# Kernel tuning notes

Hardware: AMD Instinct MI355X
Metric: run time of the kernel (lower is better)

## Reference

```python
import jax, jax.numpy as jnp
import numpy as np

B, D, N_CLASSES = 8192, 256, 64
MARGIN = 0.5


def setup_inputs() -> dict:
    key = jax.random.key(0)
    k1, k2 = jax.random.split(key)
    emb = jax.random.normal(k1, (B, D), dtype=jnp.float32)
    emb = emb / jnp.linalg.norm(emb, axis=1, keepdims=True)  # module expects L2-normalised
    labels = jax.random.randint(k2, (B,), 0, N_CLASSES)
    return {"embeddings": emb, "labels": labels}


def _pairwise_dist(x):
    # torch.cdist(x, x, p=2): sqrt of clamped squared distances, safe at 0 for grads
    sq = jnp.sum(x * x, axis=1)
    d2 = jnp.maximum(sq[:, None] + sq[None, :] - 2.0 * (x @ x.T), 0.0)
    safe = jnp.where(d2 > 0.0, d2, 1.0)
    return jnp.where(d2 > 0.0, jnp.sqrt(safe), 0.0)


def reference(embeddings, labels):
    # Vectorized semi-hard mining: for each anchor,
    #   d_ap = max positive distance; the mined negative is the MIN negative
    #   distance (argmin over the semi-hard subset == global neg argmin when
    #   that min is < d_ap + margin; otherwise the subset is empty -> skip).
    dist = _pairwise_dist(embeddings)            # [B, B]
    n = labels.shape[0]
    same = labels[:, None] == labels[None, :]
    eye = jnp.eye(n, dtype=bool)
    pos_mask = same & ~eye
    neg_mask = ~same

    NEG = jnp.float32(-1e30)
    POS = jnp.float32(1e30)
    d_ap = jnp.max(jnp.where(pos_mask, dist, NEG), axis=1)   # hardest positive
    d_an = jnp.min(jnp.where(neg_mask, dist, POS), axis=1)   # closest negative

    has_pos = jnp.any(pos_mask, axis=1)
    has_neg = jnp.any(neg_mask, axis=1)
    valid = has_pos & has_neg & (d_an < d_ap + MARGIN)       # semi-hard exists

    losses = jax.nn.relu(d_ap - d_an + MARGIN)
    count = jnp.sum(valid)
    total = jnp.sum(jnp.where(valid, losses, 0.0))
    zero = jnp.sum(embeddings) * 0.0
    return jnp.where(count > 0, total / jnp.maximum(count, 1).astype(losses.dtype), zero)
```

## Files before the change

### kernel.cpp

```cpp
#include <hip/hip_runtime.h>
#include <hip/hip_bf16.h>

#define Bn 8192
#define Dn 256
#define MARGIN_F 0.5f

typedef short short8 __attribute__((ext_vector_type(8)));
typedef float floatx4 __attribute__((ext_vector_type(4)));

__device__ inline unsigned short f2bf(float f) {
    unsigned int u = __float_as_uint(f);
    unsigned int r = (u + 0x7fffu + ((u >> 16) & 1u)) >> 16;
    return (unsigned short)r;
}

#define OFF_SQ   ((size_t)Bn * Dn * 2)
#define OFF_POS  (OFF_SQ + Bn * 4)
#define OFF_NEG  (OFF_POS + Bn * 4)
#define OFF_ACC  (OFF_NEG + Bn * 4)

__global__ __launch_bounds__(256) void prep_kernel(
        const float* __restrict__ emb, unsigned short* __restrict__ embT,
        float* __restrict__ sq, unsigned int* __restrict__ posb,
        unsigned int* __restrict__ negb, unsigned int* __restrict__ accs) {
    const int w = threadIdx.x >> 6;
    const int lane = threadIdx.x & 63;
    const int row = blockIdx.x * 4 + w;

    const float4 v = *(const float4*)(emb + (size_t)row * Dn + lane * 4);
    float ss = v.x * v.x + v.y * v.y + v.z * v.z + v.w * v.w;
    #pragma unroll
    for (int m = 32; m >= 1; m >>= 1) ss += __shfl_xor(ss, m);

    uint2 o;
    o.x = (unsigned int)f2bf(v.x) | ((unsigned int)f2bf(v.y) << 16);
    o.y = (unsigned int)f2bf(v.z) | ((unsigned int)f2bf(v.w) << 16);
    const int kg = lane >> 1;
    *(uint2*)(embT + ((size_t)kg * Bn + row) * 8 + (lane & 1) * 4) = o;

    if (lane == 0) {
        sq[row] = ss;
        posb[row] = 0u;
        negb[row] = 0xFFFFFFFFu;
    }
    if (blockIdx.x == 0 && threadIdx.x == 0) {
        accs[0] = 0u; accs[1] = 0u; accs[2] = 0u;
    }
}

__global__ __launch_bounds__(256, 3) void mine_kernel(
        const unsigned short* __restrict__ embT, const float* __restrict__ sq,
        const int* __restrict__ labels, unsigned int* __restrict__ posb,
        unsigned int* __restrict__ negb) {
    const int tid  = threadIdx.x;
    const int w    = tid >> 6;
    const int lane = tid & 63;
    const int quad = lane >> 4;
    const int c    = lane & 15;

    const int iBase = blockIdx.x * 128 + w * 32;
    const int jBase = blockIdx.y * 512;

    const size_t KS = (size_t)4 * Bn * 8;

    __shared__ __align__(16) unsigned short Bt[2][32 * 32 * 8];
    __shared__ float sqJ[512];
    __shared__ int   labJ[512];

    short8 aFrag[2][8];
    #pragma unroll
    for (int m = 0; m < 2; ++m) {
        const unsigned short* ap = embT + ((size_t)quad * Bn + iBase + m * 16 + c) * 8;
        #pragma unroll
        for (int ks = 0; ks < 8; ++ks)
            aFrag[m][ks] = *(const short8*)(ap + ks * KS);
    }
    #pragma unroll
    for (int m = 0; m < 2; ++m)
        #pragma unroll
        for (int ks = 0; ks < 8; ++ks)
            asm volatile("" : "+v"(aFrag[m][ks]));

    int labI[2][4];
    #pragma unroll
    for (int m = 0; m < 2; ++m)
        #pragma unroll
        for (int r = 0; r < 4; ++r)
            labI[m][r] = labels[iBase + m * 16 + quad * 4 + r];

    float rpos[2][4], rneg[2][4];
    #pragma unroll
    for (int m = 0; m < 2; ++m)
        #pragma unroll
        for (int r = 0; r < 4; ++r) { rpos[m][r] = -1e30f; rneg[m][r] = 1e30f; }

    {
        const int t2 = tid * 2;
        *(float2*)&sqJ[t2] = *(const float2*)&sq[jBase + t2];
        *(int2*)&labJ[t2]  = *(const int2*)&labels[jBase + t2];
    }

    const unsigned short* sbase = embT + ((size_t)(tid >> 5) * Bn + jBase + (tid & 31)) * 8;

    #define STAGE(BUF, JT) do {                                                        \
        const unsigned short* _s = sbase + (size_t)(JT) * 32 * 8;                      \
        unsigned short* _d = &Bt[BUF][(size_t)tid * 8];                                \
        _Pragma("unroll")                                                              \
        for (int cc = 0; cc < 4; ++cc)                                                 \
            __builtin_amdgcn_global_load_lds(                                          \
                (const __attribute__((address_space(1))) unsigned int*)                \
                    (_s + (size_t)cc * 8 * Bn * 8),                                    \
                (__attribute__((address_space(3))) unsigned int*)(_d + cc * 256 * 8),  \
                16, 0, 0);                                                             \
    } while (0)

    STAGE(0, 0);
    __syncthreads();

    for (int jt = 0; jt < 16; ++jt) {
        if (jt + 1 < 16) STAGE((jt + 1) & 1, jt + 1);
        const unsigned short* bt = Bt[jt & 1];
        #pragma unroll
        for (int n = 0; n < 2; ++n) {
            const int jc = jt * 32 + n * 16 + c;
            const float sj = sqJ[jc];
            const int   lj = labJ[jc];
            floatx4 acc0 = {0.f, 0.f, 0.f, 0.f};
            floatx4 acc1 = {0.f, 0.f, 0.f, 0.f};
            #pragma unroll
            for (int ks = 0; ks < 8; ++ks) {
                short8 bF = *(const short8*)(bt +
                    (size_t)((ks * 4 + quad) * 32 + n * 16 + c) * 8);
                acc0 = __builtin_amdgcn_mfma_f32_16x16x32_bf16(aFrag[0][ks], bF, acc0, 0, 0, 0);
                acc1 = __builtin_amdgcn_mfma_f32_16x16x32_bf16(aFrag[1][ks], bF, acc1, 0, 0, 0);
            }
            #pragma unroll
            for (int r = 0; r < 4; ++r) {
                float s0 = fmaf(-2.0f, acc0[r], sj);
                bool  e0 = (lj == labI[0][r]);
                rpos[0][r] = e0 ? fmaxf(rpos[0][r], s0) : rpos[0][r];
                rneg[0][r] = e0 ? rneg[0][r] : fminf(rneg[0][r], s0);
                float s1 = fmaf(-2.0f, acc1[r], sj);
                bool  e1 = (lj == labI[1][r]);
                rpos[1][r] = e1 ? fmaxf(rpos[1][r], s1) : rpos[1][r];
                rneg[1][r] = e1 ? rneg[1][r] : fminf(rneg[1][r], s1);
            }
        }
        __syncthreads();
    }
    #undef STAGE

    #pragma unroll
    for (int m = 0; m < 2; ++m)
        #pragma unroll
        for (int r = 0; r < 4; ++r) {
            float p = rpos[m][r], q = rneg[m][r];
            #pragma unroll
            for (int msk = 1; msk <= 8; msk <<= 1) {
                p = fmaxf(p, __shfl_xor(p, msk));
                q = fminf(q, __shfl_xor(q, msk));
            }
            if (c == 0) {
                int ig = iBase + m * 16 + quad * 4 + r;
                if (p > -1e29f) atomicMax(&posb[ig], __float_as_uint(p + 4.0f));
                if (q <  1e29f) atomicMin(&negb[ig], __float_as_uint(q + 4.0f));
            }
        }
}

__global__ __launch_bounds__(256) void finalize_kernel(
        const float* __restrict__ sq, const unsigned int* __restrict__ posb,
        const unsigned int* __restrict__ negb, float* __restrict__ accsF,
        unsigned int* __restrict__ accsU, float* __restrict__ out) {
    const int i = blockIdx.x * 256 + threadIdx.x;
    unsigned int pb = posb[i], nb = negb[i];
    bool hp = (pb != 0u);
    bool hn = (nb != 0xFFFFFFFFu);
    float si  = sq[i];
    float dap = sqrtf(fmaxf(si + (__uint_as_float(pb) - 4.0f), 0.0f));
    float dan = sqrtf(fmaxf(si + (__uint_as_float(nb) - 4.0f), 0.0f));
    bool valid = hp && hn && (dan < dap + MARGIN_F);
    float t  = valid ? fmaxf(dap - dan + MARGIN_F, 0.0f) : 0.0f;
    float cc = valid ? 1.0f : 0.0f;
    #pragma unroll
    for (int m = 32; m >= 1; m >>= 1) {
        t  += __shfl_xor(t, m);
        cc += __shfl_xor(cc, m);
    }
    __shared__ float sT[4], sC[4];
    int w = threadIdx.x >> 6, lane = threadIdx.x & 63;
    if (lane == 0) { sT[w] = t; sC[w] = cc; }
    __syncthreads();
    if (threadIdx.x == 0) {
        atomicAdd(&accsF[0], sT[0] + sT[1] + sT[2] + sT[3]);
        atomicAdd(&accsF[1], sC[0] + sC[1] + sC[2] + sC[3]);
        __threadfence();
        unsigned int ticket = atomicAdd(&accsU[2], 1u);
        if (ticket == gridDim.x - 1) {
            float tot = atomicAdd(&accsF[0], 0.0f);
            float cnt = atomicAdd(&accsF[1], 0.0f);
            out[0] = (cnt > 0.0f) ? tot / cnt : 0.0f;
        }
    }
}

extern "C" void kernel_launch(void* const* d_in, const int* in_sizes, int n_in,
                              void* d_out, int out_size, void* d_ws, size_t ws_size,
                              hipStream_t stream) {
    const float* emb   = (const float*)d_in[0];
    const int*  labels = (const int*)d_in[1];
    float* out = (float*)d_out;

    char* ws = (char*)d_ws;
    unsigned short* embT = (unsigned short*)ws;
    float*        sqv  = (float*)(ws + OFF_SQ);
    unsigned int* posb = (unsigned int*)(ws + OFF_POS);
    unsigned int* negb = (unsigned int*)(ws + OFF_NEG);
    float*        accsF = (float*)(ws + OFF_ACC);
    unsigned int* accsU = (unsigned int*)(ws + OFF_ACC);

    prep_kernel<<<Bn / 4, 256, 0, stream>>>(emb, embT, sqv, posb, negb, accsU);
    mine_kernel<<<dim3(64, 16), 256, 0, stream>>>(embT, sqv, labels, posb, negb);
    finalize_kernel<<<Bn / 256, 256, 0, stream>>>(sqv, posb, negb, accsF, accsU, out);
}
```

Measured before the change: 104.7 us.

## Coalesce prep transpose via LDS and remap mine blocks for XCD locality

The prep kernel now handles 32 rows per block. It stages the bf16 rows in a rotated LDS buffer and then writes embT as coalesced 16-byte chunks instead of scattered 8-byte stores. The mine kernel switches to a 1D grid and remaps block IDs so that each XCD works on a contiguous 4x2 tile region of the i/j space, which should improve L2 reuse of A and B panels. The costs are an extra LDS round trip plus a syncthreads in prep, and a fixed remapping that assumes 8 XCDs.

```diff
diff --git a/kernel.cpp b/kernel.cpp
--- a/kernel.cpp
+++ b/kernel.cpp
@@ -23,28 +23,45 @@
         const float* __restrict__ emb, unsigned short* __restrict__ embT,
         float* __restrict__ sq, unsigned int* __restrict__ posb,
         unsigned int* __restrict__ negb, unsigned int* __restrict__ accs) {
-    const int w = threadIdx.x >> 6;
-    const int lane = threadIdx.x & 63;
-    const int row = blockIdx.x * 4 + w;
-
-    const float4 v = *(const float4*)(emb + (size_t)row * Dn + lane * 4);
-    float ss = v.x * v.x + v.y * v.y + v.z * v.z + v.w * v.w;
-    #pragma unroll
-    for (int m = 32; m >= 1; m >>= 1) ss += __shfl_xor(ss, m);
-
-    uint2 o;
-    o.x = (unsigned int)f2bf(v.x) | ((unsigned int)f2bf(v.y) << 16);
-    o.y = (unsigned int)f2bf(v.z) | ((unsigned int)f2bf(v.w) << 16);
-    const int kg = lane >> 1;
-    *(uint2*)(embT + ((size_t)kg * Bn + row) * 8 + (lane & 1) * 4) = o;
-
-    if (lane == 0) {
-        sq[row] = ss;
-        posb[row] = 0u;
-        negb[row] = 0xFFFFFFFFu;
-    }
-    if (blockIdx.x == 0 && threadIdx.x == 0) {
-        accs[0] = 0u; accs[1] = 0u; accs[2] = 0u;
+    const int t    = threadIdx.x;
+    const int w    = t >> 6;
+    const int lane = t & 63;
+    const int rBase = blockIdx.x * 32;
+
+    __shared__ uint2 ldsR[32][64];
+
+    #pragma unroll
+    for (int rr = 0; rr < 8; ++rr) {
+        const int r   = w * 8 + rr;
+        const int row = rBase + r;
+        const float4 v = *(const float4*)(emb + (size_t)row * Dn + lane * 4);
+        float ss = v.x * v.x + v.y * v.y + v.z * v.z + v.w * v.w;
+        #pragma unroll
+        for (int m = 32; m >= 1; m >>= 1) ss += __shfl_xor(ss, m);
+        uint2 o;
+        o.x = (unsigned int)f2bf(v.x) | ((unsigned int)f2bf(v.y) << 16);
+        o.y = (unsigned int)f2bf(v.z) | ((unsigned int)f2bf(v.w) << 16);
+        const int cp = ((lane >> 1) + r) & 31;
+        ldsR[r][cp * 2 + (lane & 1)] = o;
+        if (lane == 0) sq[row] = ss;
+    }
+    if (t < 32) {
+        posb[rBase + t] = 0u;
+        negb[rBase + t] = 0xFFFFFFFFu;
+    }
+    if (blockIdx.x == 0 && t == 0) { accs[0] = 0u; accs[1] = 0u; accs[2] = 0u; }
+    __syncthreads();
+
+    #pragma unroll
+    for (int p = 0; p < 4; ++p) {
+        const int o  = p * 256 + t;
+        const int kg = o >> 5;
+        const int jr = o & 31;
+        const int cp = (kg + jr) & 31;
+        uint2 a = ldsR[jr][cp * 2 + 0];
+        uint2 b = ldsR[jr][cp * 2 + 1];
+        uint4 out4 = make_uint4(a.x, a.y, b.x, b.y);
+        *(uint4*)(embT + ((size_t)kg * Bn + rBase + jr) * 8) = out4;
     }
 }
 
@@ -58,8 +75,14 @@
     const int quad = lane >> 4;
     const int c    = lane & 15;
 
-    const int iBase = blockIdx.x * 128 + w * 32;
-    const int jBase = blockIdx.y * 512;
+    const int b   = blockIdx.x;
+    const int xcd = b & 7;
+    const int ii  = b >> 3;
+    const int bx  = (xcd & 3) * 16 + (ii & 15);
+    const int by  = (xcd >> 2) * 8 + (ii >> 4);
+
+    const int iBase = bx * 128 + w * 32;
+    const int jBase = by * 512;
 
     const size_t KS = (size_t)4 * Bn * 8;
 
@@ -219,7 +242,7 @@
     float*        accsF = (float*)(ws + OFF_ACC);
     unsigned int* accsU = (unsigned int*)(ws + OFF_ACC);
 
-    prep_kernel<<<Bn / 4, 256, 0, stream>>>(emb, embT, sqv, posb, negb, accsU);
-    mine_kernel<<<dim3(64, 16), 256, 0, stream>>>(embT, sqv, labels, posb, negb);
+    prep_kernel<<<Bn / 32, 256, 0, stream>>>(emb, embT, sqv, posb, negb, accsU);
+    mine_kernel<<<1024, 256, 0, stream>>>(embT, sqv, labels, posb, negb);
     finalize_kernel<<<Bn / 256, 256, 0, stream>>>(sqv, posb, negb, accsF, accsU, out);
 }
```

Result: slower. 107.3 us (+2.5%).
